# Optimization experiments

Measured on AMD Instinct MI355X. Metric: run time of the kernel, lower is better.

## Reference

```python
import jax, jax.numpy as jnp
import numpy as np

N_NODES = 100000
N_EDGES = 1600000
D = 64
L = 3


def setup_inputs() -> dict:
    key = jax.random.key(0)
    ks = jax.random.split(key, 6)
    x = jax.random.normal(ks[0], (N_NODES, D), dtype=jnp.float32)
    edge_index = jax.random.randint(ks[1], (2, N_EDGES), 0, N_NODES, dtype=jnp.int64)
    # Stacked SAGEConv params: lin_l (neighbor branch, with bias), lin_r (root branch, no bias)
    scale = 1.0 / np.sqrt(D)
    Wl = jax.random.normal(ks[2], (L, D, D), dtype=jnp.float32) * scale
    bl = jnp.zeros((L, D), dtype=jnp.float32)
    Wr = jax.random.normal(ks[3], (L, D, D), dtype=jnp.float32) * scale
    return {
        "x": x,
        "Wl": Wl,
        "bl": bl,
        "Wr": Wr,
        "edge_index": edge_index,
        "batch_size": N_NODES,
        "framework": 1,
    }


def reference(x, Wl, bl, Wr, edge_index, batch_size, framework):
    src, dst = edge_index[0], edge_index[1]
    n = x.shape[0]
    # in-degree for mean aggregation; isolated nodes -> divide by 1 (result stays 0)
    deg = jax.ops.segment_sum(jnp.ones((src.shape[0],), dtype=x.dtype), dst, num_segments=n)
    inv_deg = (1.0 / jnp.maximum(deg, 1.0))[:, None]  # [N,1]
    for i in range(Wl.shape[0]):
        msg = x[src]                                              # [E, D] gather
        agg = jax.ops.segment_sum(msg, dst, num_segments=n) * inv_deg  # [N, D] mean
        x = jax.nn.relu(agg @ Wl[i].T + bl[i] + x @ Wr[i].T)
    if framework:
        return x
    return x[:batch_size]
```

## Files before the change

kernel.cpp:

```cpp
#include <hip/hip_runtime.h>
#include <hip/hip_bf16.h>


#define D 64
#define KDIM 128
#define TS 64
#define ASTH 144
#define BSH 9
#define BNODES 512
#define ECHUNK 4096
#define BCAP 12288

typedef unsigned long long u64;
typedef unsigned short u16;

__device__ inline u16 f2bf(float f) {
    unsigned u = __float_as_uint(f);
    return (u16)((u + 0x7fffu + ((u >> 16) & 1u)) >> 16);
}
__device__ inline void bfx8_to_f(uint4 u, float* f) {
    f[0] = __uint_as_float(u.x << 16); f[1] = __uint_as_float(u.x & 0xffff0000u);
    f[2] = __uint_as_float(u.y << 16); f[3] = __uint_as_float(u.y & 0xffff0000u);
    f[4] = __uint_as_float(u.z << 16); f[5] = __uint_as_float(u.z & 0xffff0000u);
    f[6] = __uint_as_float(u.w << 16); f[7] = __uint_as_float(u.w & 0xffff0000u);
}


__global__ __launch_bounds__(256) void convert_x_kernel(
    const float* __restrict__ x, u16* __restrict__ xb, int total8)
{
    int i = blockIdx.x * 256 + threadIdx.x;
    if (i >= total8) return;
    float4 a = *(const float4*)(x + (size_t)i * 8);
    float4 b = *(const float4*)(x + (size_t)i * 8 + 4);
    uint4 o;
    o.x = (unsigned)f2bf(a.x) | ((unsigned)f2bf(a.y) << 16);
    o.y = (unsigned)f2bf(a.z) | ((unsigned)f2bf(a.w) << 16);
    o.z = (unsigned)f2bf(b.x) | ((unsigned)f2bf(b.y) << 16);
    o.w = (unsigned)f2bf(b.z) | ((unsigned)f2bf(b.w) << 16);
    *(uint4*)(xb + (size_t)i * 8) = o;
}


__global__ __launch_bounds__(256) void bin_kernel(
    const int* __restrict__ srcp, const int* __restrict__ dstp,
    int* __restrict__ bcnt, u64* __restrict__ staging,
    int nE, int nb)
{
    __shared__ int hist[1024];
    __shared__ int bbase[1024];
    int t = threadIdx.x;
    int e0 = blockIdx.x * ECHUNK;
    for (int i = t; i < nb; i += 256) hist[i] = 0;
    __syncthreads();
    int dcache[16];
#pragma unroll
    for (int j = 0; j < 16; ++j) {
        int e = e0 + j * 256 + t;
        int d = (e < nE) ? dstp[e] : -1;
        dcache[j] = d;
        if (d >= 0) atomicAdd(&hist[d >> BSH], 1);
    }
    __syncthreads();
    for (int i = t; i < nb; i += 256) {
        int c = hist[i];
        bbase[i] = (c > 0) ? atomicAdd(&bcnt[i], c) : 0;
        hist[i] = 0;
    }
    __syncthreads();
#pragma unroll
    for (int j = 0; j < 16; ++j) {
        int e = e0 + j * 256 + t;
        int d = dcache[j];
        if (d >= 0) {
            int b = d >> BSH;
            int pos = bbase[b] + atomicAdd(&hist[b], 1);
            u64 rec = ((u64)(unsigned)(d & (BNODES - 1)) << 32) | (unsigned)srcp[e];
            staging[(size_t)b * BCAP + pos] = rec;
        }
    }
}

__global__ __launch_bounds__(64) void scan_bcnt_kernel(
    const int* __restrict__ bcnt, int* __restrict__ bbase, int nb)
{
    int lane = threadIdx.x;
    int carry = 0;
    for (int base = 0; base < nb; base += 64) {
        int i = base + lane;
        int v = (i < nb) ? bcnt[i] : 0;
        int inc = v;
#pragma unroll
        for (int off = 1; off < 64; off <<= 1) {
            int v2 = __shfl_up(inc, off);
            if (lane >= off) inc += v2;
        }
        if (i < nb) bbase[i] = carry + (inc - v);
        carry += __shfl(inc, 63);
    }
}

__global__ __launch_bounds__(256) void bucket_build_kernel(
    const u64* __restrict__ staging, const int* __restrict__ bcnt,
    const int* __restrict__ bbase, int* __restrict__ offs,
    float* __restrict__ inv, int* __restrict__ csr, int n, int nb, int E)
{
    __shared__ int hist[BNODES];
    __shared__ int loffs[BNODES + 1];
    __shared__ int cur[BNODES];
    int b = blockIdx.x, t = threadIdx.x;
    int n0 = b << BSH;
    int nodes = min(BNODES, n - n0);
    int cnt = bcnt[b];
    int gbase = bbase[b];
    const u64* seg = staging + (size_t)b * BCAP;
    for (int i = t; i < nodes; i += 256) { hist[i] = 0; cur[i] = 0; }
    __syncthreads();
    for (int e = t; e < cnt; e += 256) atomicAdd(&hist[(int)(seg[e] >> 32)], 1);
    __syncthreads();
    if (t < 64) {
        int carry = 0;
        for (int base0 = 0; base0 < nodes; base0 += 64) {
            int i = base0 + t;
            int v = (i < nodes) ? hist[i] : 0;
            int inc = v;
#pragma unroll
            for (int off = 1; off < 64; off <<= 1) {
                int v2 = __shfl_up(inc, off);
                if (t >= off) inc += v2;
            }
            if (i < nodes) loffs[i] = carry + (inc - v);
            carry += __shfl(inc, 63);
        }
        if (t == 0) loffs[nodes] = carry;
    }
    __syncthreads();
    for (int i = t; i < nodes; i += 256) {
        offs[n0 + i] = gbase + loffs[i];
        inv[n0 + i] = 1.0f / fmaxf((float)hist[i], 1.0f);
    }
    if (b == nb - 1 && t == 0) offs[n] = E;
    for (int e = t; e < cnt; e += 256) {
        u64 rec = seg[e];
        int dl = (int)(rec >> 32);
        int sv = (int)(rec & 0xffffffffu);
        int pos = loffs[dl] + atomicAdd(&cur[dl], 1);
        csr[gbase + pos] = sv;
    }
}

__global__ void transpose_w_kernel(const float* __restrict__ Wl,
                                   const float* __restrict__ Wr,
                                   float* __restrict__ WT, int total)
{
    int idx = blockIdx.x * 256 + threadIdx.x;
    if (idx >= total) return;
    int j = idx & 63;
    int k = (idx >> 6) & (KDIM - 1);
    int l = idx >> 13;
    float v = (k < D) ? Wl[((l * D) + j) * D + k]
                      : Wr[((l * D) + j) * D + (k - D)];
    WT[idx] = v;
}


template <int WRITE_F32>
__global__ __launch_bounds__(256) void layer_kernel(
    const u16* __restrict__ xin, const int* __restrict__ offs,
    const int* __restrict__ csr, const float* __restrict__ inv,
    const float* __restrict__ WT,
    const float* __restrict__ bl,
    void* __restrict__ outp, int n)
{
    __shared__ u16 A[TS * ASTH];
    const int t = threadIdx.x, w = t >> 6, lane = t & 63;
    const int sub = lane >> 3;
    const int fl  = lane & 7;
    const int base = lane & 56;
    const int v0 = blockIdx.x * TS;

#pragma unroll
    for (int g = 0; g < 2; ++g) {
        const int r = w * 16 + g * 8 + sub;
        const int v = v0 + r;
        int s = 0, e = 0;
        float scale = 0.f;
        uint4 xv = make_uint4(0, 0, 0, 0);
        if (v < n) {
            s = offs[v];
            e = offs[v + 1];
            scale = inv[v];
            xv = *(const uint4*)(xin + (size_t)v * D + fl * 8);
        }
        float acc[8] = {};
        while (__any(s < e)) {
            int idx = 0;
            if (s + fl < e) idx = csr[s + fl];
            int cnt = e - s;
            cnt = cnt < 0 ? 0 : (cnt > 8 ? 8 : cnt);
            int idxv[8];
#pragma unroll
            for (int j = 0; j < 8; ++j) idxv[j] = __shfl(idx, base + j);
            uint4 rows[8];
#pragma unroll
            for (int j = 0; j < 8; ++j)
                rows[j] = *(const uint4*)(xin + (size_t)idxv[j] * D + fl * 8);
#pragma unroll
            for (int j = 0; j < 8; ++j) {
                float f[8];
                bfx8_to_f(rows[j], f);
                float m = (j < cnt) ? 1.f : 0.f;
#pragma unroll
                for (int q = 0; q < 8; ++q) acc[q] = fmaf(f[q], m, acc[q]);
            }
            s += 8;
        }
        uint4 o;
        o.x = (unsigned)f2bf(acc[0] * scale) | ((unsigned)f2bf(acc[1] * scale) << 16);
        o.y = (unsigned)f2bf(acc[2] * scale) | ((unsigned)f2bf(acc[3] * scale) << 16);
        o.z = (unsigned)f2bf(acc[4] * scale) | ((unsigned)f2bf(acc[5] * scale) << 16);
        o.w = (unsigned)f2bf(acc[6] * scale) | ((unsigned)f2bf(acc[7] * scale) << 16);
        *(uint4*)(&A[r * ASTH + fl * 8]) = o;
        *(uint4*)(&A[r * ASTH + D + fl * 8]) = xv;
    }
    __syncthreads();

    const int c = (t & 15) * 4;
    const int r = (t >> 4) * 4;
    float acc[4][4] = {};
    for (int k = 0; k < KDIM; k += 8) {
        float4 b[8];
#pragma unroll
        for (int kk = 0; kk < 8; ++kk)
            b[kk] = *(const float4*)(WT + (k + kk) * D + c);
#pragma unroll
        for (int rr = 0; rr < 4; ++rr) {
            uint4 au = *(const uint4*)(&A[(r + rr) * ASTH + k]);
            float a[8];
            bfx8_to_f(au, a);
#pragma unroll
            for (int kk = 0; kk < 8; ++kk) {
                acc[rr][0] = fmaf(a[kk], b[kk].x, acc[rr][0]);
                acc[rr][1] = fmaf(a[kk], b[kk].y, acc[rr][1]);
                acc[rr][2] = fmaf(a[kk], b[kk].z, acc[rr][2]);
                acc[rr][3] = fmaf(a[kk], b[kk].w, acc[rr][3]);
            }
        }
    }

    float4 bias = *(const float4*)(bl + c);
#pragma unroll
    for (int rr = 0; rr < 4; ++rr) {
        int v = v0 + r + rr;
        if (v < n) {
            float o0 = fmaxf(acc[rr][0] + bias.x, 0.f);
            float o1 = fmaxf(acc[rr][1] + bias.y, 0.f);
            float o2 = fmaxf(acc[rr][2] + bias.z, 0.f);
            float o3 = fmaxf(acc[rr][3] + bias.w, 0.f);
            if (WRITE_F32) {
                *(float4*)((float*)outp + (size_t)v * D + c) = make_float4(o0, o1, o2, o3);
            } else {
                uint2 p;
                p.x = (unsigned)f2bf(o0) | ((unsigned)f2bf(o1) << 16);
                p.y = (unsigned)f2bf(o2) | ((unsigned)f2bf(o3) << 16);
                *(uint2*)((u16*)outp + (size_t)v * D + c) = p;
            }
        }
    }
}


extern "C" void kernel_launch(void* const* d_in, const int* in_sizes, int n_in,
                              void* d_out, int out_size, void* d_ws, size_t ws_size,
                              hipStream_t stream)
{
    const float* x  = (const float*)d_in[0];
    const float* Wl = (const float*)d_in[1];
    const float* bl = (const float*)d_in[2];
    const float* Wr = (const float*)d_in[3];
    const int*   ei = (const int*)d_in[4];

    const int N = in_sizes[0] / D;
    const int E = in_sizes[4] / 2;
    const int L = in_sizes[1] / (D * D);

    const int* srcp = ei;
    const int* dstp = ei + E;

    const int nbuck = (N + BNODES - 1) >> BSH;

    char* w = (char*)d_ws;
    int* bcnt  = (int*)w;               w += 1024 * sizeof(int);
    int* bbase = (int*)w;               w += 1024 * sizeof(int);
    int* offs  = (int*)w;               w += (size_t)(N + 1) * sizeof(int);
    w = (char*)(((uintptr_t)w + 15) & ~(uintptr_t)15);
    float* inv = (float*)w;             w += (size_t)N * sizeof(float);
    w = (char*)(((uintptr_t)w + 15) & ~(uintptr_t)15);
    int* csr   = (int*)w;               w += (size_t)E * sizeof(int);
    w = (char*)(((uintptr_t)w + 15) & ~(uintptr_t)15);
    float* wt  = (float*)w;             w += (size_t)L * KDIM * D * sizeof(float);
    w = (char*)(((uintptr_t)w + 15) & ~(uintptr_t)15);
    u16* xbf0  = (u16*)w;               w += (size_t)N * D * sizeof(u16);
    w = (char*)(((uintptr_t)w + 15) & ~(uintptr_t)15);
    u16* xbf1  = (u16*)w;               w += (size_t)N * D * sizeof(u16);
    w = (char*)(((uintptr_t)w + 15) & ~(uintptr_t)15);
    u16* xbf2  = (u16*)w;               w += (size_t)N * D * sizeof(u16);
    w = (char*)(((uintptr_t)w + 15) & ~(uintptr_t)15);
    u64* staging = (u64*)w;

    hipMemsetAsync(bcnt, 0, 1024 * sizeof(int), stream);

    convert_x_kernel<<<(N * D / 8 + 255) / 256, 256, 0, stream>>>(x, xbf0, N * D / 8);
    bin_kernel<<<(E + ECHUNK - 1) / ECHUNK, 256, 0, stream>>>(srcp, dstp, bcnt, staging, E, nbuck);
    scan_bcnt_kernel<<<1, 64, 0, stream>>>(bcnt, bbase, nbuck);
    bucket_build_kernel<<<nbuck, 256, 0, stream>>>(staging, bcnt, bbase, offs, inv, csr, N, nbuck, E);

    int wtotal = L * KDIM * D;
    transpose_w_kernel<<<(wtotal + 255) / 256, 256, 0, stream>>>(Wl, Wr, wt, wtotal);

    const int nblk = (N + TS - 1) / TS;
    const u16* xcur = xbf0;
    for (int i = 0; i < L; ++i) {
        const float* WTl = wt + (size_t)i * KDIM * D;
        const float* bll = bl + (size_t)i * D;
        if (i == L - 1) {
            layer_kernel<1><<<nblk, 256, 0, stream>>>(xcur, offs, csr, inv, WTl, bll, d_out, N);
        } else {
            u16* xdst = (i & 1) ? xbf2 : xbf1;
            layer_kernel<0><<<nblk, 256, 0, stream>>>(xcur, offs, csr, inv, WTl, bll, xdst, N);
            xcur = xdst;
        }
    }
}
```

Baseline: 350.5 us.

## Use bf16 MFMA for layer GEMM, 512-thread blocks, fuse bucket scan into build

Replaces the scalar FP32 FMA GEMM in the layer kernel with bf16 MFMA 16x16x32 instructions. Weights are pre-packed into the MFMA operand layout as bf16. The block grows to 512 threads so each wave aggregates a single group of 8 nodes, and the next CSR index is prefetched during the gather. The separate scan kernel is removed: each bucket-build block sums the preceding bucket counts itself, and the bin kernel processes larger edge chunks. Weights are now rounded to bf16, which loses some precision, and each bucket block redundantly sums up to 196 prior counts.

```diff
diff --git a/kernel.cpp b/kernel.cpp
--- a/kernel.cpp
+++ b/kernel.cpp
@@ -5,14 +5,16 @@
 #define D 64
 #define KDIM 128
 #define TS 64
-#define ASTH 144
+#define ASTH 136
 #define BSH 9
 #define BNODES 512
-#define ECHUNK 4096
+#define ECHUNK 8192
 #define BCAP 12288
 
 typedef unsigned long long u64;
 typedef unsigned short u16;
+typedef __attribute__((ext_vector_type(8))) short bf16x8;
+typedef __attribute__((ext_vector_type(4))) float f32x4;
 
 __device__ inline u16 f2bf(float f) {
     unsigned u = __float_as_uint(f);
@@ -53,9 +55,9 @@
     int e0 = blockIdx.x * ECHUNK;
     for (int i = t; i < nb; i += 256) hist[i] = 0;
     __syncthreads();
-    int dcache[16];
-#pragma unroll
-    for (int j = 0; j < 16; ++j) {
+    int dcache[32];
+#pragma unroll
+    for (int j = 0; j < 32; ++j) {
         int e = e0 + j * 256 + t;
         int d = (e < nE) ? dstp[e] : -1;
         dcache[j] = d;
@@ -69,7 +71,7 @@
     }
     __syncthreads();
 #pragma unroll
-    for (int j = 0; j < 16; ++j) {
+    for (int j = 0; j < 32; ++j) {
         int e = e0 + j * 256 + t;
         int d = dcache[j];
         if (d >= 0) {
@@ -81,41 +83,30 @@
     }
 }
 
-__global__ __launch_bounds__(64) void scan_bcnt_kernel(
-    const int* __restrict__ bcnt, int* __restrict__ bbase, int nb)
-{
-    int lane = threadIdx.x;
-    int carry = 0;
-    for (int base = 0; base < nb; base += 64) {
-        int i = base + lane;
-        int v = (i < nb) ? bcnt[i] : 0;
-        int inc = v;
-#pragma unroll
-        for (int off = 1; off < 64; off <<= 1) {
-            int v2 = __shfl_up(inc, off);
-            if (lane >= off) inc += v2;
-        }
-        if (i < nb) bbase[i] = carry + (inc - v);
-        carry += __shfl(inc, 63);
-    }
-}
-
 __global__ __launch_bounds__(256) void bucket_build_kernel(
     const u64* __restrict__ staging, const int* __restrict__ bcnt,
-    const int* __restrict__ bbase, int* __restrict__ offs,
-    float* __restrict__ inv, int* __restrict__ csr, int n, int nb, int E)
+    int* __restrict__ offs, float* __restrict__ inv,
+    int* __restrict__ csr, int n, int nb, int E)
 {
     __shared__ int hist[BNODES];
     __shared__ int loffs[BNODES + 1];
     __shared__ int cur[BNODES];
+    __shared__ int sbase;
     int b = blockIdx.x, t = threadIdx.x;
     int n0 = b << BSH;
     int nodes = min(BNODES, n - n0);
     int cnt = bcnt[b];
-    int gbase = bbase[b];
     const u64* seg = staging + (size_t)b * BCAP;
+    if (t < 64) {
+        int partial = 0;
+        for (int i = t; i < b; i += 64) partial += bcnt[i];
+#pragma unroll
+        for (int off = 32; off > 0; off >>= 1) partial += __shfl_xor(partial, off);
+        if (t == 0) sbase = partial;
+    }
     for (int i = t; i < nodes; i += 256) { hist[i] = 0; cur[i] = 0; }
     __syncthreads();
+    int gbase = sbase;
     for (int e = t; e < cnt; e += 256) atomicAdd(&hist[(int)(seg[e] >> 32)], 1);
     __syncthreads();
     if (t < 64) {
@@ -149,26 +140,30 @@
     }
 }
 
-__global__ void transpose_w_kernel(const float* __restrict__ Wl,
-                                   const float* __restrict__ Wr,
-                                   float* __restrict__ WT, int total)
+__global__ void pack_w_kernel(const float* __restrict__ Wl,
+                              const float* __restrict__ Wr,
+                              u16* __restrict__ wpk, int total)
 {
     int idx = blockIdx.x * 256 + threadIdx.x;
     if (idx >= total) return;
-    int j = idx & 63;
-    int k = (idx >> 6) & (KDIM - 1);
-    int l = idx >> 13;
-    float v = (k < D) ? Wl[((l * D) + j) * D + k]
-                      : Wr[((l * D) + j) * D + (k - D)];
-    WT[idx] = v;
+    int j    = idx & 7;
+    int lane = (idx >> 3) & 63;
+    int nt   = (idx >> 9) & 3;
+    int kt   = (idx >> 11) & 3;
+    int l    = idx >> 13;
+    int k = kt * 32 + (lane >> 4) * 8 + j;
+    int n = nt * 16 + (lane & 15);
+    float v = (k < D) ? Wl[((l * D) + n) * D + k]
+                      : Wr[((l * D) + n) * D + (k - D)];
+    wpk[idx] = f2bf(v);
 }
 
 
 template <int WRITE_F32>
-__global__ __launch_bounds__(256) void layer_kernel(
+__global__ __launch_bounds__(512, 6) void layer_kernel(
     const u16* __restrict__ xin, const int* __restrict__ offs,
     const int* __restrict__ csr, const float* __restrict__ inv,
-    const float* __restrict__ WT,
+    const u16* __restrict__ wpk,
     const float* __restrict__ bl,
     void* __restrict__ outp, int n)
 {
@@ -179,91 +174,81 @@
     const int base = lane & 56;
     const int v0 = blockIdx.x * TS;
 
-#pragma unroll
-    for (int g = 0; g < 2; ++g) {
-        const int r = w * 16 + g * 8 + sub;
-        const int v = v0 + r;
-        int s = 0, e = 0;
-        float scale = 0.f;
-        uint4 xv = make_uint4(0, 0, 0, 0);
-        if (v < n) {
-            s = offs[v];
-            e = offs[v + 1];
-            scale = inv[v];
-            xv = *(const uint4*)(xin + (size_t)v * D + fl * 8);
-        }
-        float acc[8] = {};
-        while (__any(s < e)) {
-            int idx = 0;
-            if (s + fl < e) idx = csr[s + fl];
-            int cnt = e - s;
-            cnt = cnt < 0 ? 0 : (cnt > 8 ? 8 : cnt);
-            int idxv[8];
-#pragma unroll
-            for (int j = 0; j < 8; ++j) idxv[j] = __shfl(idx, base + j);
-            uint4 rows[8];
-#pragma unroll
-            for (int j = 0; j < 8; ++j)
-                rows[j] = *(const uint4*)(xin + (size_t)idxv[j] * D + fl * 8);
-#pragma unroll
-            for (int j = 0; j < 8; ++j) {
-                float f[8];
-                bfx8_to_f(rows[j], f);
-                float m = (j < cnt) ? 1.f : 0.f;
-#pragma unroll
-                for (int q = 0; q < 8; ++q) acc[q] = fmaf(f[q], m, acc[q]);
-            }
-            s += 8;
-        }
-        uint4 o;
-        o.x = (unsigned)f2bf(acc[0] * scale) | ((unsigned)f2bf(acc[1] * scale) << 16);
-        o.y = (unsigned)f2bf(acc[2] * scale) | ((unsigned)f2bf(acc[3] * scale) << 16);
-        o.z = (unsigned)f2bf(acc[4] * scale) | ((unsigned)f2bf(acc[5] * scale) << 16);
-        o.w = (unsigned)f2bf(acc[6] * scale) | ((unsigned)f2bf(acc[7] * scale) << 16);
-        *(uint4*)(&A[r * ASTH + fl * 8]) = o;
-        *(uint4*)(&A[r * ASTH + D + fl * 8]) = xv;
-    }
-    __syncthreads();
-
-    const int c = (t & 15) * 4;
-    const int r = (t >> 4) * 4;
-    float acc[4][4] = {};
-    for (int k = 0; k < KDIM; k += 8) {
-        float4 b[8];
-#pragma unroll
-        for (int kk = 0; kk < 8; ++kk)
-            b[kk] = *(const float4*)(WT + (k + kk) * D + c);
-#pragma unroll
-        for (int rr = 0; rr < 4; ++rr) {
-            uint4 au = *(const uint4*)(&A[(r + rr) * ASTH + k]);
-            float a[8];
-            bfx8_to_f(au, a);
-#pragma unroll
-            for (int kk = 0; kk < 8; ++kk) {
-                acc[rr][0] = fmaf(a[kk], b[kk].x, acc[rr][0]);
-                acc[rr][1] = fmaf(a[kk], b[kk].y, acc[rr][1]);
-                acc[rr][2] = fmaf(a[kk], b[kk].z, acc[rr][2]);
-                acc[rr][3] = fmaf(a[kk], b[kk].w, acc[rr][3]);
-            }
-        }
-    }
-
-    float4 bias = *(const float4*)(bl + c);
-#pragma unroll
-    for (int rr = 0; rr < 4; ++rr) {
-        int v = v0 + r + rr;
-        if (v < n) {
-            float o0 = fmaxf(acc[rr][0] + bias.x, 0.f);
-            float o1 = fmaxf(acc[rr][1] + bias.y, 0.f);
-            float o2 = fmaxf(acc[rr][2] + bias.z, 0.f);
-            float o3 = fmaxf(acc[rr][3] + bias.w, 0.f);
-            if (WRITE_F32) {
-                *(float4*)((float*)outp + (size_t)v * D + c) = make_float4(o0, o1, o2, o3);
-            } else {
-                uint2 p;
-                p.x = (unsigned)f2bf(o0) | ((unsigned)f2bf(o1) << 16);
-                p.y = (unsigned)f2bf(o2) | ((unsigned)f2bf(o3) << 16);
-                *(uint2*)((u16*)outp + (size_t)v * D + c) = p;
+    const int r = w * 8 + sub;
+    const int v = v0 + r;
+    int s = 0, e = 0;
+    float scale = 0.f;
+    uint4 xv = make_uint4(0, 0, 0, 0);
+    if (v < n) {
+        s = offs[v];
+        e = offs[v + 1];
+        scale = inv[v];
+        xv = *(const uint4*)(xin + (size_t)v * D + fl * 8);
+    }
+    float acc[8] = {};
+    int idx = 0;
+    if (s + fl < e) idx = csr[s + fl];
+    while (__any(s < e)) {
+        int cnt = e - s;
+        cnt = cnt < 0 ? 0 : (cnt > 8 ? 8 : cnt);
+        int idxv[8];
+#pragma unroll
+        for (int j = 0; j < 8; ++j) idxv[j] = __shfl(idx, base + j);
+        uint4 rows[8];
+#pragma unroll
+        for (int j = 0; j < 8; ++j)
+            rows[j] = *(const uint4*)(xin + (size_t)idxv[j] * D + fl * 8);
+        int s2 = s + 8;
+        idx = 0;
+        if (s2 + fl < e) idx = csr[s2 + fl];
+#pragma unroll
+        for (int j = 0; j < 8; ++j) {
+            float f[8];
+            bfx8_to_f(rows[j], f);
+            float m = (j < cnt) ? 1.f : 0.f;
+#pragma unroll
+            for (int q = 0; q < 8; ++q) acc[q] = fmaf(f[q], m, acc[q]);
+        }
+        s = s2;
+    }
+    uint4 o;
+    o.x = (unsigned)f2bf(acc[0] * scale) | ((unsigned)f2bf(acc[1] * scale) << 16);
+    o.y = (unsigned)f2bf(acc[2] * scale) | ((unsigned)f2bf(acc[3] * scale) << 16);
+    o.z = (unsigned)f2bf(acc[4] * scale) | ((unsigned)f2bf(acc[5] * scale) << 16);
+    o.w = (unsigned)f2bf(acc[6] * scale) | ((unsigned)f2bf(acc[7] * scale) << 16);
+    *(uint4*)(&A[r * ASTH + fl * 8]) = o;
+    *(uint4*)(&A[r * ASTH + D + fl * 8]) = xv;
+    __syncthreads();
+
+    const int m = lane & 15, quad = lane >> 4;
+    const int row16 = (w >> 1) * 16;
+    const int ntb = (w & 1) * 2;
+    f32x4 cacc[2];
+    cacc[0] = (f32x4){0.f, 0.f, 0.f, 0.f};
+    cacc[1] = (f32x4){0.f, 0.f, 0.f, 0.f};
+#pragma unroll
+    for (int kt = 0; kt < 4; ++kt) {
+        bf16x8 af = *(const bf16x8*)(&A[(row16 + m) * ASTH + kt * 32 + quad * 8]);
+#pragma unroll
+        for (int ntl = 0; ntl < 2; ++ntl) {
+            bf16x8 bf = *(const bf16x8*)(wpk + (size_t)((kt * 4 + ntb + ntl) * 64 + lane) * 8);
+            cacc[ntl] = __builtin_amdgcn_mfma_f32_16x16x32_bf16(af, bf, cacc[ntl], 0, 0, 0);
+        }
+    }
+#pragma unroll
+    for (int ntl = 0; ntl < 2; ++ntl) {
+        int col = (ntb + ntl) * 16 + m;
+        float bias = bl[col];
+#pragma unroll
+        for (int reg = 0; reg < 4; ++reg) {
+            int row = row16 + quad * 4 + reg;
+            int vv = v0 + row;
+            if (vv < n) {
+                float val = fmaxf(cacc[ntl][reg] + bias, 0.f);
+                if (WRITE_F32)
+                    ((float*)outp)[(size_t)vv * D + col] = val;
+                else
+                    ((u16*)outp)[(size_t)vv * D + col] = f2bf(val);
             }
         }
     }
@@ -291,14 +276,13 @@
 
     char* w = (char*)d_ws;
     int* bcnt  = (int*)w;               w += 1024 * sizeof(int);
-    int* bbase = (int*)w;               w += 1024 * sizeof(int);
     int* offs  = (int*)w;               w += (size_t)(N + 1) * sizeof(int);
     w = (char*)(((uintptr_t)w + 15) & ~(uintptr_t)15);
     float* inv = (float*)w;             w += (size_t)N * sizeof(float);
     w = (char*)(((uintptr_t)w + 15) & ~(uintptr_t)15);
     int* csr   = (int*)w;               w += (size_t)E * sizeof(int);
     w = (char*)(((uintptr_t)w + 15) & ~(uintptr_t)15);
-    float* wt  = (float*)w;             w += (size_t)L * KDIM * D * sizeof(float);
+    u16* wpk   = (u16*)w;               w += (size_t)L * 8192 * sizeof(u16);
     w = (char*)(((uintptr_t)w + 15) & ~(uintptr_t)15);
     u16* xbf0  = (u16*)w;               w += (size_t)N * D * sizeof(u16);
     w = (char*)(((uintptr_t)w + 15) & ~(uintptr_t)15);
@@ -312,22 +296,21 @@
 
     convert_x_kernel<<<(N * D / 8 + 255) / 256, 256, 0, stream>>>(x, xbf0, N * D / 8);
     bin_kernel<<<(E + ECHUNK - 1) / ECHUNK, 256, 0, stream>>>(srcp, dstp, bcnt, staging, E, nbuck);
-    scan_bcnt_kernel<<<1, 64, 0, stream>>>(bcnt, bbase, nbuck);
-    bucket_build_kernel<<<nbuck, 256, 0, stream>>>(staging, bcnt, bbase, offs, inv, csr, N, nbuck, E);
-
-    int wtotal = L * KDIM * D;
-    transpose_w_kernel<<<(wtotal + 255) / 256, 256, 0, stream>>>(Wl, Wr, wt, wtotal);
+    bucket_build_kernel<<<nbuck, 256, 0, stream>>>(staging, bcnt, offs, inv, csr, N, nbuck, E);
+
+    int wtotal = L * 8192;
+    pack_w_kernel<<<(wtotal + 255) / 256, 256, 0, stream>>>(Wl, Wr, wpk, wtotal);
 
     const int nblk = (N + TS - 1) / TS;
     const u16* xcur = xbf0;
     for (int i = 0; i < L; ++i) {
-        const float* WTl = wt + (size_t)i * KDIM * D;
+        const u16* wpl = wpk + (size_t)i * 8192;
         const float* bll = bl + (size_t)i * D;
         if (i == L - 1) {
-            layer_kernel<1><<<nblk, 256, 0, stream>>>(xcur, offs, csr, inv, WTl, bll, d_out, N);
+            layer_kernel<1><<<nblk, 512, 0, stream>>>(xcur, offs, csr, inv, wpl, bll, d_out, N);
         } else {
             u16* xdst = (i & 1) ? xbf2 : xbf1;
-            layer_kernel<0><<<nblk, 256, 0, stream>>>(xcur, offs, csr, inv, WTl, bll, xdst, N);
+            layer_kernel<0><<<nblk, 512, 0, stream>>>(xcur, offs, csr, inv, wpl, bll, xdst, N);
             xcur = xdst;
         }
     }
```

Result: faster. 298.1 us (-15.0%).
